# Performance work log

Hardware: AMD Instinct MI355X
Metric: run time of the kernel (lower is better)

Reference implementation:

```python
import jax, jax.numpy as jnp
import numpy as np

N_NODES = 100000
N_EDGES = 1600000


def _norms(src, dst, n_nodes, dtype):
    # DGL GraphConv norm='both': scale src by out-degree^{-1/2}, dst by in-degree^{-1/2}
    ones = jnp.ones((src.shape[0],), dtype=dtype)
    deg_out = jax.ops.segment_sum(ones, src, num_segments=n_nodes)
    deg_in = jax.ops.segment_sum(ones, dst, num_segments=n_nodes)
    inv_sqrt_out = jnp.where(deg_out > 0, jax.lax.rsqrt(jnp.maximum(deg_out, 1.0)), 0.0)
    inv_sqrt_in = jnp.where(deg_in > 0, jax.lax.rsqrt(jnp.maximum(deg_in, 1.0)), 0.0)
    return inv_sqrt_out, inv_sqrt_in


def _graph_conv(x, W, src, dst, inv_sqrt_out, inv_sqrt_in, n_nodes, relu):
    # norm='both': out = D_in^{-1/2} A D_out^{-1/2} x W
    h = x * inv_sqrt_out[:, None]
    h = h @ W                      # dense transform before aggregation
    msg = h[src]                   # gather messages along edges [E, F]
    agg = jax.ops.segment_sum(msg, dst, num_segments=n_nodes)
    out = agg * inv_sqrt_in[:, None]
    return jax.nn.relu(out) if relu else out


def setup_inputs() -> dict:
    key = jax.random.key(0)
    k1, k2, k3, k4, k5, k6 = jax.random.split(key, 6)
    in_dim, h_dim, out_dim = 128, 128, 64
    features = jax.random.normal(k1, (N_NODES, in_dim), dtype=jnp.float32)
    W1 = jax.random.normal(k2, (in_dim, h_dim), dtype=jnp.float32) * (1.0 / np.sqrt(in_dim))
    W2 = jax.random.normal(k3, (h_dim, h_dim), dtype=jnp.float32) * (1.0 / np.sqrt(h_dim))
    W3 = jax.random.normal(k4, (h_dim, out_dim), dtype=jnp.float32) * (1.0 / np.sqrt(h_dim))
    src = jax.random.randint(k5, (N_EDGES,), 0, N_NODES, dtype=jnp.int32)
    dst = jax.random.randint(k6, (N_EDGES,), 0, N_NODES, dtype=jnp.int32)
    return {"features": features, "W1": W1, "W2": W2, "W3": W3, "src": src, "dst": dst}


def reference(features, W1, W2, W3, src, dst):
    inv_sqrt_out, inv_sqrt_in = _norms(src, dst, N_NODES, features.dtype)
    h = _graph_conv(features, W1, src, dst, inv_sqrt_out, inv_sqrt_in, N_NODES, relu=True)
    h = _graph_conv(h, W2, src, dst, inv_sqrt_out, inv_sqrt_in, N_NODES, relu=True)
    h = _graph_conv(h, W3, src, dst, inv_sqrt_out, inv_sqrt_in, N_NODES, relu=False)
    return h
```

## Files before the change

kernel.cpp:

```cpp
#include <hip/hip_runtime.h>


typedef float f32x4 __attribute__((ext_vector_type(4)));
typedef __bf16 bf16x8 __attribute__((ext_vector_type(8)));

constexpr int CAP = 5120;
constexpr int MAXNB = 400;

__device__ inline unsigned short f2bf_bits(float f) {
    unsigned u = __float_as_uint(f);
    unsigned r = u + 0x7fff + ((u >> 16) & 1);
    return (unsigned short)(r >> 16);
}
__device__ inline float bf_bits2f(unsigned short s) {
    return __uint_as_float(((unsigned)s) << 16);
}
__device__ inline float bf_lo(unsigned v) { return __uint_as_float(v << 16); }
__device__ inline float bf_hi(unsigned v) { return __uint_as_float(v & 0xffff0000u); }


__global__ __launch_bounds__(512) void bucket_scatter(
    const int* __restrict__ src, const int* __restrict__ dst,
    int* __restrict__ cur_d, int* __restrict__ cur_s,
    int* __restrict__ bpair, int* __restrict__ bsrc, int E, int NB) {
    __shared__ int hd[MAXNB], hs[MAXNB], bd[MAXNB], bs[MAXNB];
    const int tid = threadIdx.x;
    for (int i = tid; i < NB; i += 512) { hd[i] = 0; hs[i] = 0; }
    __syncthreads();

    const int base = (blockIdx.x * 512 + tid) * 8;
    int s[8], d[8], rd[8], rs[8];
    bool va[8];
    if (base + 8 <= E) {
        const int4 s0 = *(const int4*)(src + base);
        const int4 s1 = *(const int4*)(src + base + 4);
        const int4 d0 = *(const int4*)(dst + base);
        const int4 d1 = *(const int4*)(dst + base + 4);
        s[0] = s0.x; s[1] = s0.y; s[2] = s0.z; s[3] = s0.w;
        s[4] = s1.x; s[5] = s1.y; s[6] = s1.z; s[7] = s1.w;
        d[0] = d0.x; d[1] = d0.y; d[2] = d0.z; d[3] = d0.w;
        d[4] = d1.x; d[5] = d1.y; d[6] = d1.z; d[7] = d1.w;
#pragma unroll
        for (int j = 0; j < 8; ++j) va[j] = true;
    } else {
#pragma unroll
        for (int j = 0; j < 8; ++j) {
            const int e = base + j;
            va[j] = e < E;
            const int ec = va[j] ? e : 0;
            s[j] = src[ec];
            d[j] = dst[ec];
        }
    }
#pragma unroll
    for (int j = 0; j < 8; ++j) {
        if (va[j]) {
            rd[j] = atomicAdd(&hd[d[j] >> 8], 1);
            rs[j] = atomicAdd(&hs[s[j] >> 8], 1);
        }
    }
    __syncthreads();
    for (int i = tid; i < NB; i += 512) {
        bd[i] = hd[i] ? atomicAdd(&cur_d[i], hd[i]) : 0;
        bs[i] = hs[i] ? atomicAdd(&cur_s[i], hs[i]) : 0;
    }
    __syncthreads();
#pragma unroll
    for (int j = 0; j < 8; ++j) {
        if (va[j]) {
            const int b = d[j] >> 8;
            const int pos = bd[b] + rd[j];
            if (pos < CAP) bpair[(size_t)b * CAP + pos] = (s[j] << 8) | (d[j] & 255);
            const int c = s[j] >> 8;
            const int ps = bs[c] + rs[j];
            if (ps < CAP) bsrc[(size_t)c * CAP + ps] = s[j];
        }
    }
}

__global__ __launch_bounds__(512) void bucket_scan(
    const int* __restrict__ cur_d, int* __restrict__ bbase, int NB) {
    __shared__ int s[512];
    const int tid = threadIdx.x;
    s[tid] = (tid < NB) ? cur_d[tid] : 0;
    __syncthreads();
    for (int off = 1; off < 512; off <<= 1) {
        int v = (tid >= off) ? s[tid - off] : 0;
        __syncthreads();
        s[tid] += v;
        __syncthreads();
    }
    if (tid < NB) bbase[tid] = (tid > 0) ? s[tid - 1] : 0;
}

__global__ __launch_bounds__(256) void csr_from_buckets(
    const int* __restrict__ bpair, const int* __restrict__ bcnt,
    const int* __restrict__ bbase, int* __restrict__ row_ptr,
    int* __restrict__ col, float* __restrict__ isi, int N, int NB) {
    __shared__ int h[256], sc[256], cur[256];
    const int b = blockIdx.x;
    const int tid = threadIdx.x;
    const int cnt = min(bcnt[b], CAP);
    const int base = bbase[b];
    const int* pairs = bpair + (size_t)b * CAP;
    h[tid] = 0;
    __syncthreads();
    for (int i = tid; i < cnt; i += 256) atomicAdd(&h[pairs[i] & 255], 1);
    __syncthreads();
    sc[tid] = h[tid];
    __syncthreads();
    for (int off = 1; off < 256; off <<= 1) {
        int v = (tid >= off) ? sc[tid - off] : 0;
        __syncthreads();
        sc[tid] += v;
        __syncthreads();
    }
    const int lp = sc[tid] - h[tid];
    const int node = b * 256 + tid;
    if (node < N) {
        row_ptr[node] = base + lp;
        isi[node] = (h[tid] > 0) ? rsqrtf((float)h[tid]) : 0.f;
    }
    if (b == NB - 1 && tid == 0) row_ptr[N] = base + cnt;
    cur[tid] = lp;
    __syncthreads();
    for (int i = tid; i < cnt; i += 256) {
        const int p = pairs[i];
        const int pos = base + atomicAdd(&cur[p & 255], 1);
        col[pos] = p >> 8;
    }
}

__global__ __launch_bounds__(256) void outdeg_buckets(
    const int* __restrict__ bsrc, const int* __restrict__ scnt,
    float* __restrict__ iso, int N) {
    __shared__ int h[256];
    const int b = blockIdx.x;
    const int tid = threadIdx.x;
    const int cnt = min(scnt[b], CAP);
    const int* vals = bsrc + (size_t)b * CAP;
    h[tid] = 0;
    __syncthreads();
    for (int i = tid; i < cnt; i += 256) atomicAdd(&h[vals[i] & 255], 1);
    __syncthreads();
    const int node = b * 256 + tid;
    if (node < N) iso[node] = (h[tid] > 0) ? rsqrtf((float)h[tid]) : 0.f;
}


__global__ __launch_bounds__(256) void wpack_kernel(
    const float* __restrict__ W, unsigned short* __restrict__ Wt_hi,
    unsigned short* __restrict__ Wt_lo, int F) {
    int t = blockIdx.x * 256 + threadIdx.x;
    if (t >= F * 128) return;
    int n = t >> 7, k = t & 127;
    float w = W[k * F + n];
    unsigned short hb = f2bf_bits(w);
    Wt_hi[t] = hb;
    Wt_lo[t] = f2bf_bits(w - bf_bits2f(hb));
}


template <int F>
__global__ __launch_bounds__(256) void gemm_mfma(
    const float* __restrict__ X, const unsigned short* __restrict__ Wt_hi,
    const unsigned short* __restrict__ Wt_lo, const float* __restrict__ so,
    unsigned short* __restrict__ Y, int N) {
    constexpr int NT = F / 16;
    const int wave = threadIdx.x >> 6;
    const int lane = threadIdx.x & 63;
    const int r0 = blockIdx.x * 128 + wave * 32;
    const int l15 = lane & 15;
    const int quad = lane >> 4;

    const int rowA0 = min(r0 + l15, N - 1);
    const int rowA1 = min(r0 + 16 + l15, N - 1);
    const float s0 = so[rowA0];
    const float s1 = so[rowA1];
    const float* pX0 = X + (size_t)rowA0 * 128 + quad * 8;
    const float* pX1 = X + (size_t)rowA1 * 128 + quad * 8;

    f32x4 acc0[NT], acc1[NT];
    const f32x4 z = {0.f, 0.f, 0.f, 0.f};
#pragma unroll
    for (int t = 0; t < NT; ++t) { acc0[t] = z; acc1[t] = z; }

    union AB { bf16x8 v; unsigned short u[8]; };

#pragma unroll
    for (int s = 0; s < 4; ++s) {
        const int kb = s * 32;
        AB bh[NT], bl[NT];
#pragma unroll
        for (int t = 0; t < NT; ++t) {
            const int n = t * 16 + l15;
            bh[t].v = *(const bf16x8*)(Wt_hi + n * 128 + kb + quad * 8);
            bl[t].v = *(const bf16x8*)(Wt_lo + n * 128 + kb + quad * 8);
        }
        float a[8];
        *(f32x4*)&a[0] = *(const f32x4*)(pX0 + kb);
        *(f32x4*)&a[4] = *(const f32x4*)(pX0 + kb + 4);
        AB ah, al;
#pragma unroll
        for (int j = 0; j < 8; ++j) {
            float x = a[j] * s0;
            unsigned short hb = f2bf_bits(x);
            ah.u[j] = hb;
            al.u[j] = f2bf_bits(x - bf_bits2f(hb));
        }
#pragma unroll
        for (int t = 0; t < NT; ++t) {
            acc0[t] = __builtin_amdgcn_mfma_f32_16x16x32_bf16(ah.v, bh[t].v, acc0[t], 0, 0, 0);
            acc0[t] = __builtin_amdgcn_mfma_f32_16x16x32_bf16(al.v, bh[t].v, acc0[t], 0, 0, 0);
            acc0[t] = __builtin_amdgcn_mfma_f32_16x16x32_bf16(ah.v, bl[t].v, acc0[t], 0, 0, 0);
        }
        *(f32x4*)&a[0] = *(const f32x4*)(pX1 + kb);
        *(f32x4*)&a[4] = *(const f32x4*)(pX1 + kb + 4);
#pragma unroll
        for (int j = 0; j < 8; ++j) {
            float x = a[j] * s1;
            unsigned short hb = f2bf_bits(x);
            ah.u[j] = hb;
            al.u[j] = f2bf_bits(x - bf_bits2f(hb));
        }
#pragma unroll
        for (int t = 0; t < NT; ++t) {
            acc1[t] = __builtin_amdgcn_mfma_f32_16x16x32_bf16(ah.v, bh[t].v, acc1[t], 0, 0, 0);
            acc1[t] = __builtin_amdgcn_mfma_f32_16x16x32_bf16(al.v, bh[t].v, acc1[t], 0, 0, 0);
            acc1[t] = __builtin_amdgcn_mfma_f32_16x16x32_bf16(ah.v, bl[t].v, acc1[t], 0, 0, 0);
        }
    }

#pragma unroll
    for (int t = 0; t < NT; ++t) {
#pragma unroll
        for (int r = 0; r < 4; ++r) {
            int node0 = r0 + quad * 4 + r;
            if (node0 < N) Y[(size_t)node0 * F + t * 16 + l15] = f2bf_bits(acc0[t][r]);
            int node1 = r0 + 16 + quad * 4 + r;
            if (node1 < N) Y[(size_t)node1 * F + t * 16 + l15] = f2bf_bits(acc1[t][r]);
        }
    }
}


template <bool RELU>
__global__ __launch_bounds__(256) void gather128(
    const unsigned short* __restrict__ msg, const int* __restrict__ row_ptr,
    const int* __restrict__ col, const float* __restrict__ isi,
    float* __restrict__ out, int N) {
    const int wave = (blockIdx.x * 256 + threadIdx.x) >> 6;
    const int lane = threadIdx.x & 63;
    if (wave >= N) return;
    const int start = row_ptr[wave], end = row_ptr[wave + 1];
    const unsigned* m32 = (const unsigned*)msg;

    float a0 = 0.f, a1 = 0.f, b0 = 0.f, b1 = 0.f;
    int e = start;
    const int nfull = (end - start) & ~7;
    const int efull = start + nfull;
    for (; e < efull; e += 8) {
        int c[8];
#pragma unroll
        for (int j = 0; j < 8; ++j) c[j] = col[e + j];
        unsigned v[8];
#pragma unroll
        for (int j = 0; j < 8; ++j) v[j] = m32[(size_t)c[j] * 64 + lane];
#pragma unroll
        for (int j = 0; j < 8; j += 2) {
            a0 += bf_lo(v[j]);     a1 += bf_hi(v[j]);
            b0 += bf_lo(v[j + 1]); b1 += bf_hi(v[j + 1]);
        }
    }
    const int rem = end - e;
    if (rem > 0) {
        int c[8];
#pragma unroll
        for (int j = 0; j < 8; ++j) c[j] = col[e + min(j, rem - 1)];
        unsigned v[8];
#pragma unroll
        for (int j = 0; j < 8; ++j) v[j] = m32[(size_t)c[j] * 64 + lane];
#pragma unroll
        for (int j = 0; j < 8; ++j) {
            float x0 = (j < rem) ? bf_lo(v[j]) : 0.f;
            float x1 = (j < rem) ? bf_hi(v[j]) : 0.f;
            a0 += x0; a1 += x1;
        }
    }
    const float sc = isi[wave];
    a0 = (a0 + b0) * sc;
    a1 = (a1 + b1) * sc;
    if (RELU) { a0 = fmaxf(a0, 0.f); a1 = fmaxf(a1, 0.f); }
    *(float2*)(out + (size_t)wave * 128 + lane * 2) = make_float2(a0, a1);
}

__global__ __launch_bounds__(256) void gather64(
    const unsigned short* __restrict__ msg, const int* __restrict__ row_ptr,
    const int* __restrict__ col, const float* __restrict__ isi,
    float* __restrict__ out, int N) {
    const int w = (blockIdx.x * 256 + threadIdx.x) >> 6;
    const int lane = threadIdx.x & 63;
    const int node = w * 2 + (lane >> 5);
    const int j31 = lane & 31;
    if (node >= N) return;
    const int start = row_ptr[node], end = row_ptr[node + 1];
    const unsigned* m32 = (const unsigned*)msg;

    float a0 = 0.f, a1 = 0.f, b0 = 0.f, b1 = 0.f;
    int e = start;
    const int nfull = (end - start) & ~7;
    const int efull = start + nfull;
    for (; e < efull; e += 8) {
        int c[8];
#pragma unroll
        for (int j = 0; j < 8; ++j) c[j] = col[e + j];
        unsigned v[8];
#pragma unroll
        for (int j = 0; j < 8; ++j) v[j] = m32[(size_t)c[j] * 32 + j31];
#pragma unroll
        for (int j = 0; j < 8; j += 2) {
            a0 += bf_lo(v[j]);     a1 += bf_hi(v[j]);
            b0 += bf_lo(v[j + 1]); b1 += bf_hi(v[j + 1]);
        }
    }
    const int rem = end - e;
    if (rem > 0) {
        int c[8];
#pragma unroll
        for (int j = 0; j < 8; ++j) c[j] = col[e + min(j, rem - 1)];
        unsigned v[8];
#pragma unroll
        for (int j = 0; j < 8; ++j) v[j] = m32[(size_t)c[j] * 32 + j31];
#pragma unroll
        for (int j = 0; j < 8; ++j) {
            float x0 = (j < rem) ? bf_lo(v[j]) : 0.f;
            float x1 = (j < rem) ? bf_hi(v[j]) : 0.f;
            a0 += x0; a1 += x1;
        }
    }
    const float sc = isi[node];
    *(float2*)(out + (size_t)node * 64 + j31 * 2) =
        make_float2((a0 + b0) * sc, (a1 + b1) * sc);
}


extern "C" void kernel_launch(void* const* d_in, const int* in_sizes, int n_in,
                              void* d_out, int out_size, void* d_ws, size_t ws_size,
                              hipStream_t stream) {
    const float* features = (const float*)d_in[0];
    const float* W1 = (const float*)d_in[1];
    const float* W2 = (const float*)d_in[2];
    const float* W3 = (const float*)d_in[3];
    const int* src = (const int*)d_in[4];
    const int* dst = (const int*)d_in[5];
    float* out = (float*)d_out;

    const int N = in_sizes[0] / 128;
    const int E = in_sizes[4];
    const int NB = (N + 255) >> 8;

    char* ws = (char*)d_ws;
    float* A = (float*)ws;                        ws += (size_t)N * 128 * 4;
    unsigned short* Y = (unsigned short*)ws;      ws += (size_t)N * 128 * 2;
    int* row_ptr = (int*)ws;                      ws += (size_t)(N + 1) * 4;
    int* col = (int*)ws;                          ws += (size_t)E * 4;
    float* iso = (float*)ws;                      ws += (size_t)N * 4;
    float* isi = (float*)ws;                      ws += (size_t)N * 4;
    int* cur_d = (int*)ws;                        ws += MAXNB * 4;
    int* cur_s = (int*)ws;                        ws += MAXNB * 4;
    int* bbase = (int*)ws;                        ws += MAXNB * 4;
    unsigned short* Wt1h = (unsigned short*)ws;   ws += 128 * 128 * 2;
    unsigned short* Wt1l = (unsigned short*)ws;   ws += 128 * 128 * 2;
    unsigned short* Wt2h = (unsigned short*)ws;   ws += 128 * 128 * 2;
    unsigned short* Wt2l = (unsigned short*)ws;   ws += 128 * 128 * 2;
    unsigned short* Wt3h = (unsigned short*)ws;   ws += 64 * 128 * 2;
    unsigned short* Wt3l = (unsigned short*)ws;

    int* bpair = (int*)A;
    int* bsrc = (int*)((char*)A + (size_t)MAXNB * CAP * 4);

    wpack_kernel<<<(128 * 128 + 255) / 256, 256, 0, stream>>>(W1, Wt1h, Wt1l, 128);
    wpack_kernel<<<(128 * 128 + 255) / 256, 256, 0, stream>>>(W2, Wt2h, Wt2l, 128);
    wpack_kernel<<<(64 * 128 + 255) / 256, 256, 0, stream>>>(W3, Wt3h, Wt3l, 64);
    hipMemsetAsync(cur_d, 0, 2 * MAXNB * sizeof(int), stream);
    const int gBS = (E + 4095) / 4096;
    bucket_scatter<<<gBS, 512, 0, stream>>>(src, dst, cur_d, cur_s, bpair, bsrc, E, NB);
    bucket_scan<<<1, 512, 0, stream>>>(cur_d, bbase, NB);
    csr_from_buckets<<<NB, 256, 0, stream>>>(bpair, cur_d, bbase, row_ptr, col, isi, N, NB);
    outdeg_buckets<<<NB, 256, 0, stream>>>(bsrc, cur_s, iso, N);

    const int gG = (N + 127) / 128;
    const int ga128 = (N * 64 + 255) / 256;
    const int ga64 = ((N / 2 + 1) * 64 + 255) / 256;

    gemm_mfma<128><<<gG, 256, 0, stream>>>(features, Wt1h, Wt1l, iso, Y, N);
    gather128<true><<<ga128, 256, 0, stream>>>(Y, row_ptr, col, isi, A, N);
    gemm_mfma<128><<<gG, 256, 0, stream>>>(A, Wt2h, Wt2l, iso, Y, N);
    gather128<true><<<ga128, 256, 0, stream>>>(Y, row_ptr, col, isi, A, N);
    gemm_mfma<64><<<gG, 256, 0, stream>>>(A, Wt3h, Wt3l, iso, Y, N);
    gather64<<<ga64, 256, 0, stream>>>(Y, row_ptr, col, isi, out, N);
}
```

Baseline: 427.8 us.

## Store hidden activations as bf16 with pre-folded out-degree scale; merge setup kernels

The gather kernels for layers 1 and 2 now fold the next layer's out-degree norm into a combined scale (in-degree times out-degree) and write bf16 activations instead of fp32. A new GEMM variant reads these bf16 activations directly and drops the hi/lo split on A and the per-row scaling. The out-degree histogram is merged into the CSR build kernel and the three weight-pack launches are merged into one. This halves activation write and read traffic and removes launches, at the cost of rounding activations to bf16, which loses the error compensation the old hi/lo split on A gave.

After: 414.0 us. -3.2%, faster.

```diff
diff --git a/kernel.cpp b/kernel.cpp
--- a/kernel.cpp
+++ b/kernel.cpp
@@ -93,19 +93,25 @@
     if (tid < NB) bbase[tid] = (tid > 0) ? s[tid - 1] : 0;
 }
 
-__global__ __launch_bounds__(256) void csr_from_buckets(
-    const int* __restrict__ bpair, const int* __restrict__ bcnt,
+__global__ __launch_bounds__(256) void csr_outdeg(
+    const int* __restrict__ bpair, const int* __restrict__ bsrc,
+    const int* __restrict__ bcnt_d, const int* __restrict__ bcnt_s,
     const int* __restrict__ bbase, int* __restrict__ row_ptr,
-    int* __restrict__ col, float* __restrict__ isi, int N, int NB) {
-    __shared__ int h[256], sc[256], cur[256];
+    int* __restrict__ col, float* __restrict__ isi, float* __restrict__ iso,
+    float* __restrict__ fscale, int N, int NB) {
+    __shared__ int h[256], hs[256], sc[256], cur[256];
     const int b = blockIdx.x;
     const int tid = threadIdx.x;
-    const int cnt = min(bcnt[b], CAP);
+    const int cnt = min(bcnt_d[b], CAP);
+    const int scnt = min(bcnt_s[b], CAP);
     const int base = bbase[b];
     const int* pairs = bpair + (size_t)b * CAP;
+    const int* svals = bsrc + (size_t)b * CAP;
     h[tid] = 0;
+    hs[tid] = 0;
     __syncthreads();
     for (int i = tid; i < cnt; i += 256) atomicAdd(&h[pairs[i] & 255], 1);
+    for (int i = tid; i < scnt; i += 256) atomicAdd(&hs[svals[i] & 255], 1);
     __syncthreads();
     sc[tid] = h[tid];
     __syncthreads();
@@ -119,7 +125,11 @@
     const int node = b * 256 + tid;
     if (node < N) {
         row_ptr[node] = base + lp;
-        isi[node] = (h[tid] > 0) ? rsqrtf((float)h[tid]) : 0.f;
+        const float di = (h[tid] > 0) ? rsqrtf((float)h[tid]) : 0.f;
+        const float dw = (hs[tid] > 0) ? rsqrtf((float)hs[tid]) : 0.f;
+        isi[node] = di;
+        iso[node] = dw;
+        fscale[node] = di * dw;
     }
     if (b == NB - 1 && tid == 0) row_ptr[N] = base + cnt;
     cur[tid] = lp;
@@ -131,33 +141,30 @@
     }
 }
 
-__global__ __launch_bounds__(256) void outdeg_buckets(
-    const int* __restrict__ bsrc, const int* __restrict__ scnt,
-    float* __restrict__ iso, int N) {
-    __shared__ int h[256];
-    const int b = blockIdx.x;
-    const int tid = threadIdx.x;
-    const int cnt = min(scnt[b], CAP);
-    const int* vals = bsrc + (size_t)b * CAP;
-    h[tid] = 0;
-    __syncthreads();
-    for (int i = tid; i < cnt; i += 256) atomicAdd(&h[vals[i] & 255], 1);
-    __syncthreads();
-    const int node = b * 256 + tid;
-    if (node < N) iso[node] = (h[tid] > 0) ? rsqrtf((float)h[tid]) : 0.f;
-}
-
-
-__global__ __launch_bounds__(256) void wpack_kernel(
-    const float* __restrict__ W, unsigned short* __restrict__ Wt_hi,
-    unsigned short* __restrict__ Wt_lo, int F) {
+
+__device__ inline void wpack1(const float* W, unsigned short* Wh,
+                              unsigned short* Wl, int t, int F) {
+    const int n = t >> 7, k = t & 127;
+    const float w = W[k * F + n];
+    const unsigned short hb = f2bf_bits(w);
+    Wh[t] = hb;
+    Wl[t] = f2bf_bits(w - bf_bits2f(hb));
+}
+
+__global__ __launch_bounds__(256) void wpack_all(
+    const float* __restrict__ W1, const float* __restrict__ W2,
+    const float* __restrict__ W3, unsigned short* __restrict__ Wt1h,
+    unsigned short* __restrict__ Wt1l, unsigned short* __restrict__ Wt2h,
+    unsigned short* __restrict__ Wt2l, unsigned short* __restrict__ Wt3h,
+    unsigned short* __restrict__ Wt3l) {
     int t = blockIdx.x * 256 + threadIdx.x;
-    if (t >= F * 128) return;
-    int n = t >> 7, k = t & 127;
-    float w = W[k * F + n];
-    unsigned short hb = f2bf_bits(w);
-    Wt_hi[t] = hb;
-    Wt_lo[t] = f2bf_bits(w - bf_bits2f(hb));
+    if (t < 16384) {
+        wpack1(W1, Wt1h, Wt1l, t, 128);
+    } else if (t < 32768) {
+        wpack1(W2, Wt2h, Wt2l, t - 16384, 128);
+    } else if (t < 40960) {
+        wpack1(W3, Wt3h, Wt3l, t - 32768, 64);
+    }
 }
 
 
@@ -244,11 +251,65 @@
 }
 
 
-template <bool RELU>
-__global__ __launch_bounds__(256) void gather128(
+template <int F>
+__global__ __launch_bounds__(256) void gemm_bf16A(
+    const unsigned short* __restrict__ A, const unsigned short* __restrict__ Wt_hi,
+    const unsigned short* __restrict__ Wt_lo, unsigned short* __restrict__ Y, int N) {
+    constexpr int NT = F / 16;
+    const int wave = threadIdx.x >> 6;
+    const int lane = threadIdx.x & 63;
+    const int r0 = blockIdx.x * 128 + wave * 32;
+    const int l15 = lane & 15;
+    const int quad = lane >> 4;
+
+    const int rowA0 = min(r0 + l15, N - 1);
+    const int rowA1 = min(r0 + 16 + l15, N - 1);
+    const unsigned short* pA0 = A + (size_t)rowA0 * 128 + quad * 8;
+    const unsigned short* pA1 = A + (size_t)rowA1 * 128 + quad * 8;
+
+    f32x4 acc0[NT], acc1[NT];
+    const f32x4 z = {0.f, 0.f, 0.f, 0.f};
+#pragma unroll
+    for (int t = 0; t < NT; ++t) { acc0[t] = z; acc1[t] = z; }
+
+#pragma unroll
+    for (int s = 0; s < 4; ++s) {
+        const int kb = s * 32;
+        bf16x8 bh[NT], bl[NT];
+#pragma unroll
+        for (int t = 0; t < NT; ++t) {
+            const int n = t * 16 + l15;
+            bh[t] = *(const bf16x8*)(Wt_hi + n * 128 + kb + quad * 8);
+            bl[t] = *(const bf16x8*)(Wt_lo + n * 128 + kb + quad * 8);
+        }
+        const bf16x8 a0 = *(const bf16x8*)(pA0 + kb);
+        const bf16x8 a1 = *(const bf16x8*)(pA1 + kb);
+#pragma unroll
+        for (int t = 0; t < NT; ++t) {
+            acc0[t] = __builtin_amdgcn_mfma_f32_16x16x32_bf16(a0, bh[t], acc0[t], 0, 0, 0);
+            acc0[t] = __builtin_amdgcn_mfma_f32_16x16x32_bf16(a0, bl[t], acc0[t], 0, 0, 0);
+            acc1[t] = __builtin_amdgcn_mfma_f32_16x16x32_bf16(a1, bh[t], acc1[t], 0, 0, 0);
+            acc1[t] = __builtin_amdgcn_mfma_f32_16x16x32_bf16(a1, bl[t], acc1[t], 0, 0, 0);
+        }
+    }
+
+#pragma unroll
+    for (int t = 0; t < NT; ++t) {
+#pragma unroll
+        for (int r = 0; r < 4; ++r) {
+            int node0 = r0 + quad * 4 + r;
+            if (node0 < N) Y[(size_t)node0 * F + t * 16 + l15] = f2bf_bits(acc0[t][r]);
+            int node1 = r0 + 16 + quad * 4 + r;
+            if (node1 < N) Y[(size_t)node1 * F + t * 16 + l15] = f2bf_bits(acc1[t][r]);
+        }
+    }
+}
+
+
+__global__ __launch_bounds__(256) void gather128_bf16(
     const unsigned short* __restrict__ msg, const int* __restrict__ row_ptr,
-    const int* __restrict__ col, const float* __restrict__ isi,
-    float* __restrict__ out, int N) {
+    const int* __restrict__ col, const float* __restrict__ fscale,
+    unsigned short* __restrict__ outA, int N) {
     const int wave = (blockIdx.x * 256 + threadIdx.x) >> 6;
     const int lane = threadIdx.x & 63;
     if (wave >= N) return;
@@ -257,8 +318,7 @@
 
     float a0 = 0.f, a1 = 0.f, b0 = 0.f, b1 = 0.f;
     int e = start;
-    const int nfull = (end - start) & ~7;
-    const int efull = start + nfull;
+    const int efull = start + ((end - start) & ~7);
     for (; e < efull; e += 8) {
         int c[8];
 #pragma unroll
@@ -282,16 +342,16 @@
         for (int j = 0; j < 8; ++j) v[j] = m32[(size_t)c[j] * 64 + lane];
 #pragma unroll
         for (int j = 0; j < 8; ++j) {
-            float x0 = (j < rem) ? bf_lo(v[j]) : 0.f;
-            float x1 = (j < rem) ? bf_hi(v[j]) : 0.f;
-            a0 += x0; a1 += x1;
-        }
-    }
-    const float sc = isi[wave];
-    a0 = (a0 + b0) * sc;
-    a1 = (a1 + b1) * sc;
-    if (RELU) { a0 = fmaxf(a0, 0.f); a1 = fmaxf(a1, 0.f); }
-    *(float2*)(out + (size_t)wave * 128 + lane * 2) = make_float2(a0, a1);
+            a0 += (j < rem) ? bf_lo(v[j]) : 0.f;
+            a1 += (j < rem) ? bf_hi(v[j]) : 0.f;
+        }
+    }
+    const float sc = fscale[wave];
+    a0 = fmaxf((a0 + b0) * sc, 0.f);
+    a1 = fmaxf((a1 + b1) * sc, 0.f);
+    const unsigned packed =
+        ((unsigned)f2bf_bits(a1) << 16) | (unsigned)f2bf_bits(a0);
+    ((unsigned*)outA)[(size_t)wave * 64 + lane] = packed;
 }
 
 __global__ __launch_bounds__(256) void gather64(
@@ -308,8 +368,7 @@
 
     float a0 = 0.f, a1 = 0.f, b0 = 0.f, b1 = 0.f;
     int e = start;
-    const int nfull = (end - start) & ~7;
-    const int efull = start + nfull;
+    const int efull = start + ((end - start) & ~7);
     for (; e < efull; e += 8) {
         int c[8];
 #pragma unroll
@@ -333,9 +392,8 @@
         for (int j = 0; j < 8; ++j) v[j] = m32[(size_t)c[j] * 32 + j31];
 #pragma unroll
         for (int j = 0; j < 8; ++j) {
-            float x0 = (j < rem) ? bf_lo(v[j]) : 0.f;
-            float x1 = (j < rem) ? bf_hi(v[j]) : 0.f;
-            a0 += x0; a1 += x1;
+            a0 += (j < rem) ? bf_lo(v[j]) : 0.f;
+            a1 += (j < rem) ? bf_hi(v[j]) : 0.f;
         }
     }
     const float sc = isi[node];
@@ -360,12 +418,13 @@
     const int NB = (N + 255) >> 8;
 
     char* ws = (char*)d_ws;
-    float* A = (float*)ws;                        ws += (size_t)N * 128 * 4;
+    unsigned short* A = (unsigned short*)ws;      ws += (size_t)N * 128 * 2;
     unsigned short* Y = (unsigned short*)ws;      ws += (size_t)N * 128 * 2;
     int* row_ptr = (int*)ws;                      ws += (size_t)(N + 1) * 4;
     int* col = (int*)ws;                          ws += (size_t)E * 4;
     float* iso = (float*)ws;                      ws += (size_t)N * 4;
     float* isi = (float*)ws;                      ws += (size_t)N * 4;
+    float* fscale = (float*)ws;                   ws += (size_t)N * 4;
     int* cur_d = (int*)ws;                        ws += MAXNB * 4;
     int* cur_s = (int*)ws;                        ws += MAXNB * 4;
     int* bbase = (int*)ws;                        ws += MAXNB * 4;
@@ -374,29 +433,27 @@
     unsigned short* Wt2h = (unsigned short*)ws;   ws += 128 * 128 * 2;
     unsigned short* Wt2l = (unsigned short*)ws;   ws += 128 * 128 * 2;
     unsigned short* Wt3h = (unsigned short*)ws;   ws += 64 * 128 * 2;
-    unsigned short* Wt3l = (unsigned short*)ws;
+    unsigned short* Wt3l = (unsigned short*)ws;   ws += 64 * 128 * 2;
 
     int* bpair = (int*)A;
     int* bsrc = (int*)((char*)A + (size_t)MAXNB * CAP * 4);
 
-    wpack_kernel<<<(128 * 128 + 255) / 256, 256, 0, stream>>>(W1, Wt1h, Wt1l, 128);
-    wpack_kernel<<<(128 * 128 + 255) / 256, 256, 0, stream>>>(W2, Wt2h, Wt2l, 128);
-    wpack_kernel<<<(64 * 128 + 255) / 256, 256, 0, stream>>>(W3, Wt3h, Wt3l, 64);
+    wpack_all<<<160, 256, 0, stream>>>(W1, W2, W3, Wt1h, Wt1l, Wt2h, Wt2l, Wt3h, Wt3l);
     hipMemsetAsync(cur_d, 0, 2 * MAXNB * sizeof(int), stream);
     const int gBS = (E + 4095) / 4096;
     bucket_scatter<<<gBS, 512, 0, stream>>>(src, dst, cur_d, cur_s, bpair, bsrc, E, NB);
     bucket_scan<<<1, 512, 0, stream>>>(cur_d, bbase, NB);
-    csr_from_buckets<<<NB, 256, 0, stream>>>(bpair, cur_d, bbase, row_ptr, col, isi, N, NB);
-    outdeg_buckets<<<NB, 256, 0, stream>>>(bsrc, cur_s, iso, N);
+    csr_outdeg<<<NB, 256, 0, stream>>>(bpair, bsrc, cur_d, cur_s, bbase, row_ptr,
+                                       col, isi, iso, fscale, N, NB);
 
     const int gG = (N + 127) / 128;
     const int ga128 = (N * 64 + 255) / 256;
     const int ga64 = ((N / 2 + 1) * 64 + 255) / 256;
 
     gemm_mfma<128><<<gG, 256, 0, stream>>>(features, Wt1h, Wt1l, iso, Y, N);
-    gather128<true><<<ga128, 256, 0, stream>>>(Y, row_ptr, col, isi, A, N);
-    gemm_mfma<128><<<gG, 256, 0, stream>>>(A, Wt2h, Wt2l, iso, Y, N);
-    gather128<true><<<ga128, 256, 0, stream>>>(Y, row_ptr, col, isi, A, N);
-    gemm_mfma<64><<<gG, 256, 0, stream>>>(A, Wt3h, Wt3l, iso, Y, N);
+    gather128_bf16<<<ga128, 256, 0, stream>>>(Y, row_ptr, col, fscale, A, N);
+    gemm_bf16A<128><<<gG, 256, 0, stream>>>(A, Wt2h, Wt2l, Y, N);
+    gather128_bf16<<<ga128, 256, 0, stream>>>(Y, row_ptr, col, fscale, A, N);
+    gemm_bf16A<64><<<gG, 256, 0, stream>>>(A, Wt3h, Wt3l, Y, N);
     gather64<<<ga64, 256, 0, stream>>>(Y, row_ptr, col, isi, out, N);
 }
```
